# Optimization experiments

Hardware: AMD Instinct MI355X
Metric: run time of the kernel (lower is better)

## Reference

```python
import jax, jax.numpy as jnp
import numpy as np

N_NODES = 100000
IN_CH, HID_CH, OUT_CH = 128, 64, 8
N_EDGES = 3200000


def gcn_conv(x, src, dst, W, b, n):
    # PyG GCNConv: linear transform, add self-loops, symmetric deg^-1/2
    # normalization, scatter-add aggregation at target nodes, then bias.
    h = x @ W                                   # [N, out]
    loop = jnp.arange(n)
    s = jnp.concatenate([src, loop])            # [E+N]
    d = jnp.concatenate([dst, loop])
    deg = jax.ops.segment_sum(jnp.ones_like(d, h.dtype), d, num_segments=n)
    dinv = jnp.where(deg > 0, jax.lax.rsqrt(deg), 0.0)
    norm = dinv[s] * dinv[d]                    # [E+N]
    msgs = norm[:, None] * h[s]                 # gather + scale, [E+N, out]
    out = jax.ops.segment_sum(msgs, d, num_segments=n)  # scatter-add
    return out + b


def setup_inputs() -> dict:
    key = jax.random.key(0)
    k1, k2, k3, k4, k5, k6 = jax.random.split(key, 6)
    x = jax.random.normal(k1, (N_NODES, IN_CH), dtype=jnp.float32)
    edge_index = jax.random.randint(k2, (2, N_EDGES), 0, N_NODES, dtype=jnp.int64)
    # Glorot-style init for the two GCNConv layers
    W1 = jax.random.normal(k3, (IN_CH, HID_CH), dtype=jnp.float32) / np.sqrt(IN_CH)
    b1 = jnp.zeros((HID_CH,), dtype=jnp.float32)
    W2 = jax.random.normal(k4, (HID_CH, OUT_CH), dtype=jnp.float32) / np.sqrt(HID_CH)
    b2 = jnp.zeros((OUT_CH,), dtype=jnp.float32)
    return {"x": x, "edge_index": edge_index, "W1": W1, "b1": b1, "W2": W2, "b2": b2}


def reference(x, edge_index, W1, b1, W2, b2):
    n = x.shape[0]
    src, dst = edge_index[0], edge_index[1]
    h = gcn_conv(x, src, dst, W1, b1, n)
    h = jax.nn.relu(h)
    h = gcn_conv(h, src, dst, W2, b2, n)
    return jax.nn.log_softmax(h, axis=1)
```

## Files before the change

### kernel.cpp

```cpp
#include <hip/hip_runtime.h>
#include <hip/hip_fp16.h>
#include <hip/hip_fp8.h>

#define IN_CH  128
#define HID_CH 64
#define OUT_CH 8
#define BSH    8
#define BCAP   8960
#define PCHUNK 8192
#define LDK    136

typedef unsigned long long ull;
typedef float floatx2 __attribute__((ext_vector_type(2)));
typedef _Float16 f16x8 __attribute__((ext_vector_type(8)));
typedef float f32x4 __attribute__((ext_vector_type(4)));


__device__ __forceinline__ unsigned char f2fp8(float f) {
    __hip_fp8_e4m3 t(f);
    return (unsigned char)t.__x;
}
__device__ __forceinline__ float fp82f(unsigned char b) {
    __hip_fp8_e4m3 t;
    t.__x = (__hip_fp8_storage_t)b;
    return (float)t;
}

__device__ __forceinline__ void acc8(float* acc, ull p) {
#if __has_builtin(__builtin_amdgcn_cvt_pk_f32_fp8)
    unsigned lo = (unsigned)p, hi = (unsigned)(p >> 32);
    floatx2 q0 = __builtin_amdgcn_cvt_pk_f32_fp8(lo, false);
    floatx2 q1 = __builtin_amdgcn_cvt_pk_f32_fp8(lo, true);
    floatx2 q2 = __builtin_amdgcn_cvt_pk_f32_fp8(hi, false);
    floatx2 q3 = __builtin_amdgcn_cvt_pk_f32_fp8(hi, true);
    acc[0] += q0.x; acc[1] += q0.y; acc[2] += q1.x; acc[3] += q1.y;
    acc[4] += q2.x; acc[5] += q2.y; acc[6] += q3.x; acc[7] += q3.y;
#else
#pragma unroll
    for (int j = 0; j < 8; ++j) acc[j] += fp82f((unsigned char)(p >> (8 * j)));
#endif
}

__global__ __launch_bounds__(512) void part_k(const int* __restrict__ ei, int E, int NB,
                                              int* __restrict__ gcnt,
                                              unsigned* __restrict__ bucket) {
    __shared__ int cnt[512];
    __shared__ int scn[512];
    __shared__ int gbase[512];
    __shared__ unsigned ordered[PCHUNK];
    int t = threadIdx.x;
    int c0 = blockIdx.x * PCHUNK;
    const int* __restrict__ src = ei;
    const int* __restrict__ dst = ei + E;

    cnt[t] = 0;
    __syncthreads();
    for (int i = t; i < PCHUNK; i += 512) {
        int e = c0 + i;
        if (e < E) atomicAdd(&cnt[dst[e] >> BSH], 1);
    }
    __syncthreads();
    scn[t] = cnt[t];
    __syncthreads();
    for (int o = 1; o < 512; o <<= 1) {
        int v = (t >= o) ? scn[t - o] : 0;
        __syncthreads();
        scn[t] += v;
        __syncthreads();
    }
    int ex = scn[t] - cnt[t];
    __syncthreads();
    scn[t] = ex;
    int cn = cnt[t];
    gbase[t] = (t < NB && cn > 0) ? atomicAdd(&gcnt[t], cn) : 0;
    __syncthreads();
    cnt[t] = 0;
    __syncthreads();
    for (int i = t; i < PCHUNK; i += 512) {
        int e = c0 + i;
        if (e < E) {
            int s = src[e], d = dst[e];
            int k = d >> BSH;
            int slot = scn[k] + atomicAdd(&cnt[k], 1);
            ordered[slot] = (unsigned)s | ((unsigned)(d & 255) << 24);
        }
    }
    __syncthreads();
    int tot = scn[511] + cnt[511];
    for (int i = t; i < tot; i += 512) {
        int lo = 0, hi = 512;
        #pragma unroll
        for (int it = 0; it < 10; ++it) {
            int mid = (lo + hi) >> 1;
            if (scn[mid] > i) hi = mid; else lo = mid + 1;
        }
        int k = lo - 1;
        bucket[(size_t)k * BCAP + gbase[k] + (i - scn[k])] = ordered[i];
    }
}

__global__ __launch_bounds__(256) void sort_k(unsigned* __restrict__ bucket,
                                              const int* __restrict__ gcnt,
                                              int* __restrict__ deg,
                                              float* __restrict__ dinv,
                                              int* __restrict__ off, int n) {
    __shared__ int cnt[256];
    __shared__ int excl[256];
    __shared__ int cur[256];
    __shared__ int ordered[BCAP];
    int bk = blockIdx.x;
    int t = threadIdx.x;
    int node0 = bk << BSH;
    cnt[t] = 0;
    __syncthreads();
    int ecnt = gcnt[bk];
    unsigned* __restrict__ bb = bucket + (size_t)bk * BCAP;
    for (int i = t; i < ecnt; i += 256) {
        unsigned p = bb[i];
        atomicAdd(&cnt[p >> 24], 1);
    }
    __syncthreads();
    int dg = cnt[t];
    excl[t] = dg;
    __syncthreads();
    for (int o = 1; o < 256; o <<= 1) {
        int v = (t >= o) ? excl[t - o] : 0;
        __syncthreads();
        excl[t] += v;
        __syncthreads();
    }
    int ex = excl[t] - dg;
    __syncthreads();
    excl[t] = ex;
    cur[t] = 0;
    int node = node0 + t;
    if (node < n) {
        deg[node]  = dg;
        dinv[node] = rsqrtf((float)dg + 1.0f);
        off[node]  = bk * BCAP + ex;
    }
    __syncthreads();
    for (int i = t; i < ecnt; i += 256) {
        unsigned p = bb[i];
        int s = (int)(p & 0xFFFFFFu), d = (int)(p >> 24);
        int slot = excl[d] + atomicAdd(&cur[d], 1);
        ordered[slot] = s;
    }
    __syncthreads();
    int* __restrict__ csr = (int*)bb;
    for (int i = t; i < ecnt; i += 256) csr[i] = ordered[i];
}

__global__ __launch_bounds__(256) void gemm1_k(const float* __restrict__ x,
                                               const float* __restrict__ W,
                                               const float* __restrict__ dinv,
                                               unsigned char* __restrict__ h, int n) {
    __shared__ __align__(16) float uShared[64 * 68];
    __shared__ __align__(16) _Float16 Wt[64 * LDK];
    int t = threadIdx.x;
    int node0 = blockIdx.x * 64;
    _Float16* xs = (_Float16*)uShared;

    for (int i = t; i < 64 * 32; i += 256) {
        int row = i >> 5, c4 = i & 31;
        int node = node0 + row;
        float4 v = (node < n) ? *(const float4*)(x + (size_t)node * IN_CH + c4 * 4)
                              : make_float4(0.f, 0.f, 0.f, 0.f);
        _Float16* dstp = xs + row * LDK + c4 * 4;
        dstp[0] = (_Float16)v.x; dstp[1] = (_Float16)v.y;
        dstp[2] = (_Float16)v.z; dstp[3] = (_Float16)v.w;
    }
    for (int i = t; i < IN_CH * HID_CH; i += 256) {
        int k = i >> 6, nn = i & 63;
        Wt[nn * LDK + k] = (_Float16)W[i];
    }
    __syncthreads();

    int w = t >> 6, lane = t & 63;
    int rsel = lane & 15, ksel = lane >> 4;
    f32x4 acc[4];
#pragma unroll
    for (int ct = 0; ct < 4; ++ct) acc[ct] = (f32x4){0.f, 0.f, 0.f, 0.f};

#pragma unroll
    for (int kk = 0; kk < 4; ++kk) {
        f16x8 a = *(const f16x8*)(xs + (16 * w + rsel) * LDK + kk * 32 + ksel * 8);
#pragma unroll
        for (int ct = 0; ct < 4; ++ct) {
            f16x8 b = *(const f16x8*)(Wt + (ct * 16 + rsel) * LDK + kk * 32 + ksel * 8);
            acc[ct] = __builtin_amdgcn_mfma_f32_16x16x32_f16(a, b, acc[ct], 0, 0, 0);
        }
    }
    __syncthreads();
    float* outS = uShared;
#pragma unroll
    for (int ct = 0; ct < 4; ++ct)
#pragma unroll
        for (int r = 0; r < 4; ++r)
            outS[(16 * w + ksel * 4 + r) * 68 + ct * 16 + rsel] = acc[ct][r];
    __syncthreads();

    {
        int row = t >> 2, quad = t & 3;
        int node = node0 + row;
        if (node < n) {
            float dv = dinv[node];
            const float* srcp = outS + row * 68 + quad * 16;
            unsigned un[4];
#pragma unroll
            for (int g = 0; g < 4; ++g) {
                unsigned v = 0;
#pragma unroll
                for (int j = 0; j < 4; ++j)
                    v |= (unsigned)f2fp8(srcp[g * 4 + j] * dv) << (8 * j);
                un[g] = v;
            }
            *(uint4*)(h + (size_t)node * HID_CH + quad * 16) = make_uint4(un[0], un[1], un[2], un[3]);
        }
    }
}

__global__ __launch_bounds__(256) void agg1_gather_k(const int* __restrict__ off,
                                                     const int* __restrict__ deg,
                                                     const int* __restrict__ csr,
                                                     const float* __restrict__ dinv,
                                                     const unsigned char* __restrict__ h,
                                                     const float* __restrict__ b1,
                                                     __half* __restrict__ z, int n) {
    int tid = threadIdx.x;
    int node = blockIdx.x * 4 + (tid >> 6);
    if (node >= n) return;
    int lane = tid & 63;
    int e8 = lane >> 3, cg = lane & 7;

    float acc[8];
#pragma unroll
    for (int j = 0; j < 8; ++j) acc[j] = 0.0f;

    if (e8 == 0)
        acc8(acc, *(const ull*)(h + (size_t)node * HID_CH + cg * 8));

    int o = off[node], end = o + deg[node];
    int i = o + e8;
    for (; i + 24 < end; i += 32) {
        int s0 = csr[i], s1 = csr[i + 8], s2 = csr[i + 16], s3 = csr[i + 24];
        ull p0 = *(const ull*)(h + (size_t)s0 * HID_CH + cg * 8);
        ull p1 = *(const ull*)(h + (size_t)s1 * HID_CH + cg * 8);
        ull p2 = *(const ull*)(h + (size_t)s2 * HID_CH + cg * 8);
        ull p3 = *(const ull*)(h + (size_t)s3 * HID_CH + cg * 8);
        acc8(acc, p0); acc8(acc, p1); acc8(acc, p2); acc8(acc, p3);
    }
    for (; i < end; i += 8)
        acc8(acc, *(const ull*)(h + (size_t)csr[i] * HID_CH + cg * 8));

#pragma unroll
    for (int j = 0; j < 8; ++j) {
        acc[j] += __shfl_xor(acc[j], 8);
        acc[j] += __shfl_xor(acc[j], 16);
        acc[j] += __shfl_xor(acc[j], 32);
    }

    if (e8 == 0) {
        float dv = dinv[node];
        union { __half2 hv[4]; uint4 u; } pk;
#pragma unroll
        for (int j2 = 0; j2 < 4; ++j2) {
            float z0 = fmaxf(dv * acc[2 * j2]      + b1[cg * 8 + 2 * j2],     0.0f);
            float z1v = fmaxf(dv * acc[2 * j2 + 1] + b1[cg * 8 + 2 * j2 + 1], 0.0f);
            pk.hv[j2] = __floats2half2_rn(z0, z1v);
        }
        *(uint4*)(z + (size_t)node * HID_CH + cg * 8) = pk.u;
    }
}

__global__ __launch_bounds__(256) void gemm2_k(const __half* __restrict__ z,
                                               const float* __restrict__ W,
                                               const float* __restrict__ dinv,
                                               __half* __restrict__ h2, int n) {
    __shared__ float Ws[HID_CH * OUT_CH];
    int tid = threadIdx.x;
    for (int i = tid; i < HID_CH * OUT_CH; i += 256) Ws[i] = W[i];
    __syncthreads();
    int node = blockIdx.x * 256 + tid;
    if (node >= n) return;
    float acc[OUT_CH];
#pragma unroll
    for (int c = 0; c < OUT_CH; ++c) acc[c] = 0.0f;
    const __half2* zr = (const __half2*)(z + (size_t)node * HID_CH);
#pragma unroll 8
    for (int k2 = 0; k2 < HID_CH / 2; ++k2) {
        float2 v = __half22float2(zr[k2]);
        int k = k2 * 2;
#pragma unroll
        for (int c = 0; c < OUT_CH; ++c)
            acc[c] += v.x * Ws[k * OUT_CH + c] + v.y * Ws[(k + 1) * OUT_CH + c];
    }
    float dv = dinv[node];
    __half2* o2 = (__half2*)(h2 + (size_t)node * OUT_CH);
#pragma unroll
    for (int c2 = 0; c2 < OUT_CH / 2; ++c2)
        o2[c2] = __floats2half2_rn(dv * acc[2 * c2], dv * acc[2 * c2 + 1]);
}

__global__ __launch_bounds__(256) void agg2_final_k(const int* __restrict__ off,
                                                    const int* __restrict__ deg,
                                                    const int* __restrict__ csr,
                                                    const float* __restrict__ dinv,
                                                    const __half* __restrict__ h2,
                                                    const float* __restrict__ b,
                                                    float* __restrict__ out, int n) {
    int tid = threadIdx.x;
    int node = blockIdx.x * 32 + (tid >> 3);
    int c = tid & 7;
    if (node >= n) return;
    float dv = dinv[node];
    int o = off[node], dg = deg[node];
    float a0 = 0, a1 = 0, a2 = 0, a3 = 0;
    int i = o, end = o + dg;
    for (; i + 3 < end; i += 4) {
        int s0 = csr[i], s1 = csr[i + 1], s2 = csr[i + 2], s3 = csr[i + 3];
        a0 += __half2float(h2[(size_t)s0 * OUT_CH + c]);
        a1 += __half2float(h2[(size_t)s1 * OUT_CH + c]);
        a2 += __half2float(h2[(size_t)s2 * OUT_CH + c]);
        a3 += __half2float(h2[(size_t)s3 * OUT_CH + c]);
    }
    for (; i < end; ++i) a0 += __half2float(h2[(size_t)csr[i] * OUT_CH + c]);
    float self = __half2float(h2[(size_t)node * OUT_CH + c]);
    float val = dv * ((a0 + a1) + (a2 + a3) + self) + b[c];
    float m = val;
    m = fmaxf(m, __shfl_xor(m, 1, 8));
    m = fmaxf(m, __shfl_xor(m, 2, 8));
    m = fmaxf(m, __shfl_xor(m, 4, 8));
    float s8 = expf(val - m);
    s8 += __shfl_xor(s8, 1, 8);
    s8 += __shfl_xor(s8, 2, 8);
    s8 += __shfl_xor(s8, 4, 8);
    out[(size_t)node * OUT_CH + c] = val - m - logf(s8);
}

extern "C" void kernel_launch(void* const* d_in, const int* in_sizes, int n_in,
                              void* d_out, int out_size, void* d_ws, size_t ws_size,
                              hipStream_t stream) {
    const float* x  = (const float*)d_in[0];
    const int*   ei = (const int*)d_in[1];
    const float* W1 = (const float*)d_in[2];
    const float* b1 = (const float*)d_in[3];
    const float* W2 = (const float*)d_in[4];
    const float* b2 = (const float*)d_in[5];
    float* out = (float*)d_out;

    const int n = in_sizes[0] / IN_CH;
    const int E = in_sizes[1] / 2;
    const int NP = 100352;
    const int NB = (n + 255) >> BSH;

    int*      deg    = (int*)d_ws;
    float*    dinv   = (float*)(deg + NP);
    int*      gcnt   = (int*)(dinv + NP);
    int*      off    = gcnt + 512;
    unsigned* bucket = (unsigned*)(off + NP);
    unsigned char* h1 = (unsigned char*)(bucket + (size_t)NB * BCAP);
    __half*   z1     = (__half*)(h1 + (size_t)NP * HID_CH);
    __half*   h2     = z1 + (size_t)NP * HID_CH;
    int*      csr    = (int*)bucket;

    const int NCH = (E + PCHUNK - 1) / PCHUNK;

    hipMemsetAsync(gcnt, 0, 512 * sizeof(int), stream);
    part_k<<<NCH, 512, 0, stream>>>(ei, E, NB, gcnt, bucket);
    sort_k<<<NB, 256, 0, stream>>>(bucket, gcnt, deg, dinv, off, n);
    gemm1_k<<<(n + 63) / 64, 256, 0, stream>>>(x, W1, dinv, h1, n);
    agg1_gather_k<<<(n + 3) / 4, 256, 0, stream>>>(off, deg, csr, dinv, h1, b1, z1, n);
    gemm2_k<<<(n + 255) / 256, 256, 0, stream>>>(z1, W2, dinv, h2, n);
    agg2_final_k<<<(n + 31) / 32, 256, 0, stream>>>(off, deg, csr, dinv, h2, b2, out, n);
}
```

Measured before the change: 166.2 us.

## Store bucket ids in partition, widen gemm1 blocks, edge-parallel layer-2 gather

The partition kernel now records each edge's bucket id in shared memory, so the scatter pass no longer runs a binary search over the prefix sums. gemm1 processes 128 nodes per 512-thread block instead of 64 per 256. The final aggregation switches from one thread per channel to 16 threads per node: each thread loads whole 16-byte fp16 rows for a strided subset of edges, and the partial sums are combined with shuffles before one lane computes log-softmax and writes vectorized output. The aim is fewer, wider memory transactions and less per-edge index work. The cost is extra shared memory in the partition kernel and a larger shared-memory footprint in gemm1; the rest of gemm1's body is not shown, so it is unclear whether it correctly indexes the extra rows at 512 threads.

```diff
diff --git a/kernel.cpp b/kernel.cpp
--- a/kernel.cpp
+++ b/kernel.cpp
@@ -8,7 +8,6 @@
 #define BSH    8
 #define BCAP   8960
 #define PCHUNK 8192
-#define LDK    136
 
 typedef unsigned long long ull;
 typedef float floatx2 __attribute__((ext_vector_type(2)));
@@ -48,6 +47,7 @@
     __shared__ int scn[512];
     __shared__ int gbase[512];
     __shared__ unsigned ordered[PCHUNK];
+    __shared__ unsigned short ordK[PCHUNK];
     int t = threadIdx.x;
     int c0 = blockIdx.x * PCHUNK;
     const int* __restrict__ src = ei;
@@ -83,18 +83,13 @@
             int k = d >> BSH;
             int slot = scn[k] + atomicAdd(&cnt[k], 1);
             ordered[slot] = (unsigned)s | ((unsigned)(d & 255) << 24);
+            ordK[slot] = (unsigned short)k;
         }
     }
     __syncthreads();
     int tot = scn[511] + cnt[511];
     for (int i = t; i < tot; i += 512) {
-        int lo = 0, hi = 512;
-        #pragma unroll
-        for (int it = 0; it < 10; ++it) {
-            int mid = (lo + hi) >> 1;
-            if (scn[mid] > i) hi = mid; else lo = mid + 1;
-        }
-        int k = lo - 1;
+        int k = ordK[i];
         bucket[(size_t)k * BCAP + gbase[k] + (i - scn[k])] = ordered[i];
     }
 }
@@ -151,17 +146,18 @@
     for (int i = t; i < ecnt; i += 256) csr[i] = ordered[i];
 }
 
-__global__ __launch_bounds__(256) void gemm1_k(const float* __restrict__ x,
+#define LDK 136
+__global__ __launch_bounds__(512) void gemm1_k(const float* __restrict__ x,
                                                const float* __restrict__ W,
                                                const float* __restrict__ dinv,
                                                unsigned char* __restrict__ h, int n) {
-    __shared__ __align__(16) float uShared[64 * 68];
+    __shared__ __align__(16) float uShared[128 * 68];
     __shared__ __align__(16) _Float16 Wt[64 * LDK];
     int t = threadIdx.x;
-    int node0 = blockIdx.x * 64;
+    int node0 = blockIdx.x * 128;
     _Float16* xs = (_Float16*)uShared;
 
-    for (int i = t; i < 64 * 32; i += 256) {
+    for (int i = t; i < 128 * 32; i += 512) {
         int row = i >> 5, c4 = i & 31;
         int node = node0 + row;
         float4 v = (node < n) ? *(const float4*)(x + (size_t)node * IN_CH + c4 * 4)
@@ -170,7 +166,7 @@
         dstp[0] = (_Float16)v.x; dstp[1] = (_Float16)v.y;
         dstp[2] = (_Float16)v.z; dstp[3] = (_Float16)v.w;
     }
-    for (int i = t; i < IN_CH * HID_CH; i += 256) {
+    for (int i = t; i < IN_CH * HID_CH; i += 512) {
         int k = i >> 6, nn = i & 63;
         Wt[nn * LDK + k] = (_Float16)W[i];
     }
@@ -310,32 +306,73 @@
                                                     const float* __restrict__ b,
                                                     float* __restrict__ out, int n) {
     int tid = threadIdx.x;
-    int node = blockIdx.x * 32 + (tid >> 3);
-    int c = tid & 7;
+    int node = blockIdx.x * 16 + (tid >> 4);
     if (node >= n) return;
-    float dv = dinv[node];
-    int o = off[node], dg = deg[node];
-    float a0 = 0, a1 = 0, a2 = 0, a3 = 0;
-    int i = o, end = o + dg;
-    for (; i + 3 < end; i += 4) {
-        int s0 = csr[i], s1 = csr[i + 1], s2 = csr[i + 2], s3 = csr[i + 3];
-        a0 += __half2float(h2[(size_t)s0 * OUT_CH + c]);
-        a1 += __half2float(h2[(size_t)s1 * OUT_CH + c]);
-        a2 += __half2float(h2[(size_t)s2 * OUT_CH + c]);
-        a3 += __half2float(h2[(size_t)s3 * OUT_CH + c]);
-    }
-    for (; i < end; ++i) a0 += __half2float(h2[(size_t)csr[i] * OUT_CH + c]);
-    float self = __half2float(h2[(size_t)node * OUT_CH + c]);
-    float val = dv * ((a0 + a1) + (a2 + a3) + self) + b[c];
-    float m = val;
-    m = fmaxf(m, __shfl_xor(m, 1, 8));
-    m = fmaxf(m, __shfl_xor(m, 2, 8));
-    m = fmaxf(m, __shfl_xor(m, 4, 8));
-    float s8 = expf(val - m);
-    s8 += __shfl_xor(s8, 1, 8);
-    s8 += __shfl_xor(s8, 2, 8);
-    s8 += __shfl_xor(s8, 4, 8);
-    out[(size_t)node * OUT_CH + c] = val - m - logf(s8);
+    int s16 = tid & 15;
+
+    float acc[8];
+#pragma unroll
+    for (int c = 0; c < 8; ++c) acc[c] = 0.0f;
+
+    auto addrow = [&](const __half* rp) {
+        uint4 u = *(const uint4*)rp;
+        union { uint4 u; __half2 hv[4]; } cv; cv.u = u;
+#pragma unroll
+        for (int q = 0; q < 4; ++q) {
+            float2 f = __half22float2(cv.hv[q]);
+            acc[2 * q]     += f.x;
+            acc[2 * q + 1] += f.y;
+        }
+    };
+
+    if (s16 == 0) addrow(h2 + (size_t)node * OUT_CH);
+
+    int o = off[node], end = o + deg[node];
+    int i = o + s16;
+    for (; i + 16 < end; i += 32) {
+        int s0 = csr[i], s1 = csr[i + 16];
+        const __half* r0 = h2 + (size_t)s0 * OUT_CH;
+        const __half* r1 = h2 + (size_t)s1 * OUT_CH;
+        uint4 u0 = *(const uint4*)r0;
+        uint4 u1 = *(const uint4*)r1;
+        union { uint4 u; __half2 hv[4]; } c0, c1; c0.u = u0; c1.u = u1;
+#pragma unroll
+        for (int q = 0; q < 4; ++q) {
+            float2 f0 = __half22float2(c0.hv[q]);
+            float2 f1 = __half22float2(c1.hv[q]);
+            acc[2 * q]     += f0.x + f1.x;
+            acc[2 * q + 1] += f0.y + f1.y;
+        }
+    }
+    for (; i < end; i += 16) addrow(h2 + (size_t)csr[i] * OUT_CH);
+
+#pragma unroll
+    for (int c = 0; c < 8; ++c) {
+        acc[c] += __shfl_xor(acc[c], 1);
+        acc[c] += __shfl_xor(acc[c], 2);
+        acc[c] += __shfl_xor(acc[c], 4);
+        acc[c] += __shfl_xor(acc[c], 8);
+    }
+
+    if (s16 == 0) {
+        float dv = dinv[node];
+        float val[8];
+        float m = -1e30f;
+#pragma unroll
+        for (int c = 0; c < 8; ++c) {
+            val[c] = dv * acc[c] + b[c];
+            m = fmaxf(m, val[c]);
+        }
+        float s = 0.0f;
+#pragma unroll
+        for (int c = 0; c < 8; ++c) s += expf(val[c] - m);
+        float lse = m + logf(s);
+        float4 o0 = make_float4(val[0] - lse, val[1] - lse, val[2] - lse, val[3] - lse);
+        float4 o1 = make_float4(val[4] - lse, val[5] - lse, val[6] - lse, val[7] - lse);
+        float* op = out + (size_t)node * OUT_CH;
+        *(float4*)op = o0;
+        *(float4*)(op + 4) = o1;
+    }
 }
 
 extern "C" void kernel_launch(void* const* d_in, const int* in_sizes, int n_in,
@@ -369,8 +406,8 @@
     hipMemsetAsync(gcnt, 0, 512 * sizeof(int), stream);
     part_k<<<NCH, 512, 0, stream>>>(ei, E, NB, gcnt, bucket);
     sort_k<<<NB, 256, 0, stream>>>(bucket, gcnt, deg, dinv, off, n);
-    gemm1_k<<<(n + 63) / 64, 256, 0, stream>>>(x, W1, dinv, h1, n);
+    gemm1_k<<<(n + 127) / 128, 512, 0, stream>>>(x, W1, dinv, h1, n);
     agg1_gather_k<<<(n + 3) / 4, 256, 0, stream>>>(off, deg, csr, dinv, h1, b1, z1, n);
     gemm2_k<<<(n + 255) / 256, 256, 0, stream>>>(z1, W2, dinv, h2, n);
-    agg2_final_k<<<(n + 31) / 32, 256, 0, stream>>>(off, deg, csr, dinv, h2, b2, out, n);
-}
+    agg2_final_k<<<(n + 15) / 16, 256, 0, stream>>>(off, deg, csr, dinv, h2, b2, out, n);
+}
```

Measured after the change: 158.4 us. 4.7% less time.
